# Kernel optimization log

Measured on AMD Instinct MI355X. Metric: run time of the kernel, lower is better.

## Reference

```python
import jax, jax.numpy as jnp
import numpy as np

B, N, T, D = 8, 16, 64, 4
H = 256
N_EDGE_TYPES = 2
BN_EPS = 1e-5


def _rel_matrices(n):
    idx = np.arange(n)
    send, recv = np.meshgrid(idx, idx, indexing='ij')
    mask = send != recv
    eye = np.eye(n, dtype=np.float32)
    return jnp.asarray(eye[recv[mask]]), jnp.asarray(eye[send[mask]])


def _mlp_params(key, n_in, n_hid, n_out):
    k1, k2 = jax.random.split(key)
    s1 = (2.0 / (n_in + n_hid)) ** 0.5
    s2 = (2.0 / (n_hid + n_out)) ** 0.5
    return (jax.random.normal(k1, (n_hid, n_in)) * s1,
            jnp.full((n_hid,), 0.1),
            jax.random.normal(k2, (n_out, n_hid)) * s2,
            jnp.full((n_out,), 0.1),
            jnp.ones((n_out,)),
            jnp.zeros((n_out,)))


def setup_inputs() -> dict:
    key = jax.random.key(0)
    ks = jax.random.split(key, 12)
    rel_rec, rel_send = _rel_matrices(N)
    inp = {
        'inputs': jax.random.normal(ks[0], (B, N, T, D), dtype=jnp.float32),
        'rel_rec': rel_rec,
        'rel_send': rel_send,
    }
    for name, (ni, no), k in [('m1', (D, H), ks[1]), ('m2', (2 * H, H), ks[2]),
                              ('m3', (H, H), ks[3]), ('m4', (3 * H, H), ks[4])]:
        w1, b1, w2, b2, g, be = _mlp_params(k, ni, H, no)
        inp.update({f'{name}_w1': w1, f'{name}_b1': b1, f'{name}_w2': w2,
                    f'{name}_b2': b2, f'{name}_g': g, f'{name}_be': be})
    scale = (1.0 / H) ** 0.5
    inp['lstm_wih'] = jax.random.uniform(ks[5], (3, 4 * H, H), minval=-scale, maxval=scale)
    inp['lstm_whh'] = jax.random.uniform(ks[6], (3, 4 * H, H), minval=-scale, maxval=scale)
    inp['lstm_bih'] = jax.random.uniform(ks[7], (3, 4 * H), minval=-scale, maxval=scale)
    inp['lstm_bhh'] = jax.random.uniform(ks[8], (3, 4 * H), minval=-scale, maxval=scale)
    inp['fco_w'] = jax.random.normal(ks[9], (N_EDGE_TYPES, H)) * (2.0 / (H + N_EDGE_TYPES)) ** 0.5
    inp['fco_b'] = jnp.full((N_EDGE_TYPES,), 0.1)
    return inp


def _mlp(x, w1, b1, w2, b2, g, be):
    h = jax.nn.elu(x @ w1.T + b1)
    h = jax.nn.elu(h @ w2.T + b2)
    # BatchNorm1d (training mode, biased var) over flattened (batch, nodes/edges)
    m = h.mean(axis=(0, 1), keepdims=True)
    v = jnp.mean((h - m) ** 2, axis=(0, 1), keepdims=True)
    return (h - m) * jax.lax.rsqrt(v + BN_EPS) * g + be


def _lstm_layer(x, wih, whh, bih, bhh):
    # x: [BR, T, H]; PyTorch gate order i, f, g, o
    BR = x.shape[0]
    h0 = jnp.zeros((BR, whh.shape[1]), x.dtype)

    def step(carry, xt):
        h, c = carry
        gates = xt @ wih.T + bih + h @ whh.T + bhh
        i, f, g, o = jnp.split(gates, 4, axis=-1)
        c = jax.nn.sigmoid(f) * c + jax.nn.sigmoid(i) * jnp.tanh(g)
        h = jax.nn.sigmoid(o) * jnp.tanh(c)
        return (h, c), h

    (_, _), ys = jax.lax.scan(step, (h0, h0), jnp.swapaxes(x, 0, 1))
    return jnp.swapaxes(ys, 0, 1)


def _node2edge(x, rel_rec, rel_send):
    # rel_*: [E, N], x: [BT, N, H] -> [BT, E, 2H] with (senders, receivers)
    return jnp.concatenate([rel_send @ x, rel_rec @ x], axis=2)


def reference(inputs, rel_rec, rel_send,
              m1_w1, m1_b1, m1_w2, m1_b2, m1_g, m1_be,
              m2_w1, m2_b1, m2_w2, m2_b2, m2_g, m2_be,
              m3_w1, m3_b1, m3_w2, m3_b2, m3_g, m3_be,
              m4_w1, m4_b1, m4_w2, m4_b2, m4_g, m4_be,
              lstm_wih, lstm_whh, lstm_bih, lstm_bhh,
              fco_w, fco_b):
    b, n, t, d = inputs.shape
    x = jnp.transpose(inputs, (0, 2, 1, 3)).reshape(b * t, n, d)
    x = _mlp(x, m1_w1, m1_b1, m1_w2, m1_b2, m1_g, m1_be)          # [BT, N, H]
    x = _node2edge(x, rel_rec, rel_send)                            # [BT, E, 2H]
    x = _mlp(x, m2_w1, m2_b1, m2_w2, m2_b2, m2_g, m2_be)           # [BT, E, H]
    x_skip = x
    # edge2node: rel_rec^T x / N (intended NRI math; source has an arity bug)
    x = jnp.einsum('en,beh->bnh', rel_rec, x) / n                   # [BT, N, H]
    x = _mlp(x, m3_w1, m3_b1, m3_w2, m3_b2, m3_g, m3_be)
    x = _node2edge(x, rel_rec, rel_send)                            # [BT, E, 2H]
    x = jnp.concatenate([x, x_skip], axis=2)                        # [BT, E, 3H]
    x = _mlp(x, m4_w1, m4_b1, m4_w2, m4_b2, m4_g, m4_be)           # [BT, E, H]
    r = x.shape[1]
    x = x.reshape(b, t, r, -1).transpose(0, 2, 1, 3).reshape(b * r, t, -1)
    for layer in range(3):
        x = _lstm_layer(x, lstm_wih[layer], lstm_whh[layer],
                        lstm_bih[layer], lstm_bhh[layer])
    x = x[:, -1, :].reshape(b, r, -1)
    return (x @ fco_w.T + fco_b).reshape(b, r, fco_w.shape[0])
```

## Files before the change

### kernel.cpp

```cpp
#include <hip/hip_runtime.h>


typedef __attribute__((ext_vector_type(4))) float f32x4;
typedef __attribute__((ext_vector_type(8))) _Float16 f16x8;
typedef unsigned long long u64;

#define DEVFN static __device__ __forceinline__

DEVFN float elu_f(float x)  { return x > 0.f ? x : __expf(x) - 1.f; }
DEVFN float sig_f(float x)  { return 1.f / (1.f + __expf(-x)); }
DEVFN float tanh_f(float x) { return 1.f - 2.f / (1.f + __expf(2.f * x)); }

#define M_ID  0
#define M_N2E 1
#define M_M4  2
#define M_L0C 3
#define M_IDC 4

template<int MODE, bool DOELU>
__global__ __launch_bounds__(256) void gemmg(
    const _Float16* __restrict__ A0, const _Float16* __restrict__ A1,
    const float* __restrict__ st0, const float* __restrict__ st1,
    const int* __restrict__ sidx, const int* __restrict__ ridx,
    const _Float16* __restrict__ W, const float* __restrict__ bias,
    _Float16* __restrict__ out, int M, int O, int tc)
{
    constexpr int NSEG = (MODE == M_M4) ? 3 : ((MODE == M_N2E) ? 2 : 1);
    constexpr bool HAS_ST = (MODE == M_N2E) || (MODE == M_M4) || (MODE == M_L0C);
    const int K = NSEG * 256;

    __shared__ _Float16 As[128][40];
    __shared__ _Float16 Ws[128][40];

    const int tid  = threadIdx.x;
    const int lane = tid & 63;
    const int wv   = tid >> 6;
    const int wr   = wv >> 1, wc = wv & 1;
    const int lr   = lane & 15, kg = lane >> 4;
    const int m0   = blockIdx.x * 128;
    const int o0   = blockIdx.y * 128;
    const int srow = tid >> 1;
    const int scol = (tid & 1) * 16;

    const _Float16* ab[3] = {nullptr, nullptr, nullptr};
    const float*   stp[3] = {nullptr, nullptr, nullptr};
    {
        int r = m0 + srow;
        if constexpr (MODE == M_ID) {
            ab[0] = A0 + (size_t)r * 256;
        } else if constexpr (MODE == M_N2E) {
            int bt = r / 240, e = r - bt * 240;
            ab[0] = A0 + (size_t)(bt * 16 + sidx[e]) * 256;
            ab[1] = A0 + (size_t)(bt * 16 + ridx[e]) * 256;
            stp[0] = st0; stp[1] = st0;
        } else if constexpr (MODE == M_M4) {
            int bt = r / 240, e = r - bt * 240;
            ab[0] = A0 + (size_t)(bt * 16 + sidx[e]) * 256;
            ab[1] = A0 + (size_t)(bt * 16 + ridx[e]) * 256;
            ab[2] = A1 + (size_t)r * 256;
            stp[0] = st0; stp[1] = st0; stp[2] = st1;
        } else if constexpr (MODE == M_L0C) {
            int rr = r >> 4, tt = r & 15;
            int b = rr / 240, e = rr - b * 240;
            ab[0] = A0 + (size_t)((b * 64 + tc + tt) * 240 + e) * 256;
            stp[0] = st0;
        } else {
            ab[0] = A0 + (size_t)((r >> 4) * 64 + tc + (r & 15)) * 256;
        }
    }
    const _Float16* wrow = W + (size_t)(o0 + srow) * K;

    f32x4 acc[4][4];
#pragma unroll
    for (int i = 0; i < 4; ++i)
#pragma unroll
        for (int j = 0; j < 4; ++j) acc[i][j] = (f32x4)0.f;

#pragma unroll
    for (int seg = 0; seg < NSEG; ++seg) {
        const _Float16* asrc = ab[seg];
        const float*    st   = stp[seg];
#pragma unroll 1
        for (int kk = 0; kk < 256; kk += 32) {
            f16x8 v0 = *(const f16x8*)(asrc + kk + scol);
            f16x8 v1 = *(const f16x8*)(asrc + kk + scol + 8);
            if constexpr (HAS_ST) {
#pragma unroll
                for (int j = 0; j < 8; ++j) {
                    int c0 = kk + scol + j, c1 = c0 + 8;
                    v0[j] = (_Float16)((float)v0[j] * st[512 + c0] + st[768 + c0]);
                    v1[j] = (_Float16)((float)v1[j] * st[512 + c1] + st[768 + c1]);
                }
            }
            f16x8 w0 = *(const f16x8*)(wrow + seg * 256 + kk + scol);
            f16x8 w1 = *(const f16x8*)(wrow + seg * 256 + kk + scol + 8);
            *(f16x8*)&As[srow][scol]     = v0;
            *(f16x8*)&As[srow][scol + 8] = v1;
            *(f16x8*)&Ws[srow][scol]     = w0;
            *(f16x8*)&Ws[srow][scol + 8] = w1;
            __syncthreads();

            f16x8 af[4], bf[4];
#pragma unroll
            for (int rf = 0; rf < 4; ++rf)
                af[rf] = *(const f16x8*)&As[wr * 64 + rf * 16 + lr][kg * 8];
#pragma unroll
            for (int cf = 0; cf < 4; ++cf)
                bf[cf] = *(const f16x8*)&Ws[wc * 64 + cf * 16 + lr][kg * 8];
#pragma unroll
            for (int rf = 0; rf < 4; ++rf)
#pragma unroll
                for (int cf = 0; cf < 4; ++cf)
                    acc[rf][cf] = __builtin_amdgcn_mfma_f32_16x16x32_f16(
                        af[rf], bf[cf], acc[rf][cf], 0, 0, 0);
            __syncthreads();
        }
    }

#pragma unroll
    for (int rf = 0; rf < 4; ++rf) {
#pragma unroll
        for (int cf = 0; cf < 4; ++cf) {
            int c = o0 + wc * 64 + cf * 16 + lr;
            float bv = bias ? bias[c] : 0.f;
#pragma unroll
            for (int rg = 0; rg < 4; ++rg) {
                int r = m0 + wr * 64 + rf * 16 + kg * 4 + rg;
                float v = acc[rf][cf][rg] + bv;
                if (DOELU) v = elu_f(v);
                out[(size_t)r * O + c] = (_Float16)v;
            }
        }
    }
}

__global__ void mlp1_g1(const float* __restrict__ inp, const float* __restrict__ w1,
                        const float* __restrict__ b1, _Float16* __restrict__ out)
{
    int idx = blockIdx.x * 256 + threadIdx.x;
    int o = idx & 255, row = idx >> 8;
    int bt = row >> 4, n = row & 15, b = bt >> 6, t = bt & 63;
    const float* xp = inp + (((b * 16 + n) * 64 + t) << 2);
    const float* wp = w1 + (o << 2);
    float v = b1[o] + xp[0] * wp[0] + xp[1] * wp[1] + xp[2] * wp[2] + xp[3] * wp[3];
    out[idx] = (_Float16)elu_f(v);
}

__global__ void decode_k(const float* __restrict__ rel_rec, const float* __restrict__ rel_send,
                         int* __restrict__ sidx, int* __restrict__ ridx,
                         int* __restrict__ nodeEdges)
{
    int tid = threadIdx.x;
    if (tid < 240) {
        float as = 0.f, ar = 0.f;
        for (int n = 0; n < 16; ++n) {
            as += rel_send[tid * 16 + n] * (float)n;
            ar += rel_rec[tid * 16 + n] * (float)n;
        }
        sidx[tid] = (int)(as + 0.5f);
        ridx[tid] = (int)(ar + 0.5f);
    }
    __syncthreads();
    if (tid < 16) {
        int k = 0;
        for (int e = 0; e < 240; ++e)
            if (ridx[e] == tid) nodeEdges[tid * 15 + (k++)] = e;
    }
}

__global__ void cvt16(const float* __restrict__ src, _Float16* __restrict__ dst, int n)
{
    int i = blockIdx.x * 256 + threadIdx.x;
    if (i < n) dst[i] = (_Float16)src[i];
}

__global__ void cvtperm(const float* __restrict__ src, _Float16* __restrict__ dst)
{
    int idx = blockIdx.x * 256 + threadIdx.x;
    int k = idx & 255;
    int cp = (idx >> 8) & 1023;
    int l = idx >> 18;
    dst[idx] = (_Float16)src[((size_t)l * 1024 + (cp & 3) * 256 + (cp >> 2)) * 256 + k];
}

__global__ void wprep2(const float* __restrict__ whh, _Float16* __restrict__ W2)
{
    int idx = blockIdx.x * 256 + threadIdx.x;
    int lane = idx & 63; int u = idx >> 6;
    int kc = u & 7; u >>= 3;
    int g  = u & 3; u >>= 2;
    int w  = u & 3; u >>= 2;
    int cq = u & 3; u >>= 2;
    int l  = u;
    int gatecol = g * 256 + cq * 64 + w * 16 + (lane & 15);
    int k = kc * 32 + (lane >> 4) * 8;
    const float* src = whh + (size_t)l * 262144 + (size_t)gatecol * 256 + k;
    f16x8 v;
#pragma unroll
    for (int j = 0; j < 8; ++j) v[j] = (_Float16)src[j];
    *(f16x8*)&W2[(size_t)idx * 8] = v;
}

__global__ void bn_stats(const _Float16* __restrict__ h, float* __restrict__ stats,
                         int Mrows, int rowsPerBlk)
{
    int col = threadIdx.x;
    int r0 = blockIdx.x * rowsPerBlk;
    int r1 = r0 + rowsPerBlk; if (r1 > Mrows) r1 = Mrows;
    float s = 0.f, q = 0.f;
    for (int r = r0; r < r1; ++r) {
        float v = (float)h[(size_t)r * 256 + col];
        s += v; q += v * v;
    }
    atomicAdd(&stats[col], s);
    atomicAdd(&stats[256 + col], q);
}

__global__ void bn_fin(float* __restrict__ stats, const float* __restrict__ g,
                       const float* __restrict__ be, float invM)
{
    int c = threadIdx.x;
    float m  = stats[c] * invM;
    float vr = stats[256 + c] * invM - m * m;
    float sc = rsqrtf(vr + 1e-5f) * g[c];
    stats[512 + c] = sc;
    stats[768 + c] = be[c] - m * sc;
}

__global__ void e2n_k(const _Float16* __restrict__ x2, const float* __restrict__ st,
                      const int* __restrict__ nodeEdges, _Float16* __restrict__ out)
{
    int idx = blockIdx.x * 256 + threadIdx.x;
    int c = (idx & 31) * 8;
    int n = (idx >> 5) & 15;
    int bt = idx >> 9;
    float s[8] = {0, 0, 0, 0, 0, 0, 0, 0};
    for (int k = 0; k < 15; ++k) {
        int e = nodeEdges[n * 15 + k];
        f16x8 v = *(const f16x8*)&x2[(size_t)(bt * 240 + e) * 256 + c];
#pragma unroll
        for (int j = 0; j < 8; ++j) s[j] += (float)v[j];
    }
    f16x8 r;
#pragma unroll
    for (int j = 0; j < 8; ++j)
        r[j] = (_Float16)((st[512 + c + j] * s[j] + 15.f * st[768 + c + j]) * 0.0625f);
    *(f16x8*)&out[(size_t)(bt * 16 + n) * 256 + c] = r;
}

#define STEP(TT, XPU, XPN) do {                                                \
    const int t_ = tc + (TT);                                                  \
    const int ttn_ = ((TT) < 15) ? (TT) + 1 : 15;                              \
    _Pragma("unroll")                                                          \
    for (int rt = 0; rt < 2; ++rt)                                             \
        _Pragma("unroll")                                                      \
        for (int rg = 0; rg < 4; ++rg) {                                       \
            int row = rt * 16 + kg * 4 + rg;                                   \
            XPN[rt * 4 + rg] = *(const u64*)(xwb                               \
                + ((size_t)(r0 + row) * 16 + ttn_) * 1024);                    \
        }                                                                      \
    f32x4 acc[4][2];                                                           \
    _Pragma("unroll")                                                          \
    for (int g = 0; g < 4; ++g)                                                \
        _Pragma("unroll")                                                      \
        for (int rt = 0; rt < 2; ++rt) acc[g][rt] = (f32x4)0.f;                \
    _Pragma("unroll")                                                          \
    for (int kc = 0; kc < 8; ++kc) {                                           \
        const int kb = kc * 64 + kg * 16;                                      \
        const int o0_ = (lr * 512 + kb) ^ ((lr & 7) << 4);                     \
        const int o1_ = ((16 + lr) * 512 + kb) ^ (((16 + lr) & 7) << 4);       \
        f16x8 a0 = *(const f16x8*)(hfulb + o0_);                               \
        f16x8 a1 = *(const f16x8*)(hfulb + o1_);                               \
        _Pragma("unroll")                                                      \
        for (int g = 0; g < 4; ++g) {                                          \
            f16x8 bf = *(const f16x8*)&Wlds[(((w * 4 + g) * 8 + kc) * 64 + lane) * 8]; \
            acc[g][0] = __builtin_amdgcn_mfma_f32_16x16x32_f16(a0, bf, acc[g][0], 0, 0, 0); \
            acc[g][1] = __builtin_amdgcn_mfma_f32_16x16x32_f16(a1, bf, acc[g][1], 0, 0, 0); \
        }                                                                      \
    }                                                                          \
    __syncthreads();                                                           \
    _Float16 hv0[4], hv1[4];                                                   \
    _Pragma("unroll")                                                          \
    for (int rt = 0; rt < 2; ++rt)                                             \
        _Pragma("unroll")                                                      \
        for (int rg = 0; rg < 4; ++rg) {                                       \
            int row = rt * 16 + kg * 4 + rg;                                   \
            union { u64 u; _Float16 h[4]; } xu; xu.u = XPU[rt * 4 + rg];       \
            float gi = acc[0][rt][rg] + (float)xu.h[0] + bs[0];                \
            float gf = acc[1][rt][rg] + (float)xu.h[1] + bs[1];                \
            float gg = acc[2][rt][rg] + (float)xu.h[2] + bs[2];                \
            float go = acc[3][rt][rg] + (float)xu.h[3] + bs[3];                \
            float c  = sig_f(gf) * cst[rt][rg] + sig_f(gi) * tanh_f(gg);       \
            cst[rt][rg] = c;                                                   \
            float h = sig_f(go) * tanh_f(c);                                   \
            _Float16 h16 = (_Float16)h;                                        \
            if (rt == 0) hv0[rg] = h16; else hv1[rg] = h16;                    \
            int off = (row * 512 + col * 2) ^ ((row & 7) << 4);                \
            *(_Float16*)(hfulb + off) = h16;                                   \
        }                                                                      \
    {                                                                          \
        const int lc = w * 16 + lr;                                            \
        union { _Float16 h[4]; u64 u; } pk;                                    \
        pk.h[0] = hv0[0]; pk.h[1] = hv0[1]; pk.h[2] = hv0[2]; pk.h[3] = hv0[3];\
        u64 p0 = pk.u;                                                         \
        pk.h[0] = hv1[0]; pk.h[1] = hv1[1]; pk.h[2] = hv1[2]; pk.h[3] = hv1[3];\
        u64 p1 = pk.u;                                                         \
        u64* hb = hex + ((size_t)fid * 2 + (t_ & 1)) * 512;                    \
        __hip_atomic_store(&hb[(lc * 2 + 0) * 4 + kg], p0,                     \
                           __ATOMIC_RELAXED, __HIP_MEMORY_SCOPE_AGENT);        \
        __hip_atomic_store(&hb[(lc * 2 + 1) * 4 + kg], p1,                     \
                           __ATOMIC_RELAXED, __HIP_MEMORY_SCOPE_AGENT);        \
    }                                                                          \
    __syncthreads();                                                           \
    if (tid == 0)                                                              \
        __hip_atomic_store(&flags[fid], t_ + 1,                                \
                           __ATOMIC_RELEASE, __HIP_MEMORY_SCOPE_AGENT);        \
    if (tid < 3) {                                                             \
        int s = tid + (tid >= colq ? 1 : 0);                                   \
        while (__hip_atomic_load(&flags[rgrp * 4 + s],                         \
                 __ATOMIC_ACQUIRE, __HIP_MEMORY_SCOPE_AGENT) < t_ + 1) {}      \
    }                                                                          \
    __syncthreads();                                                           \
    _Pragma("unroll 1")                                                        \
    for (int i = tid; i < 1536; i += 256) {                                    \
        int sbi = i >> 9;                                                      \
        int sq  = sbi + (sbi >= colq ? 1 : 0);                                 \
        int idx = i & 511;                                                     \
        u64 v = __hip_atomic_load(                                             \
            &hex[(((size_t)rgrp * 4 + sq) * 2 + (t_ & 1)) * 512 + idx],        \
            __ATOMIC_RELAXED, __HIP_MEMORY_SCOPE_AGENT);                       \
        int lc = idx >> 3, rt = (idx >> 2) & 1, k4 = idx & 3;                  \
        int cg = sq * 64 + lc;                                                 \
        union { u64 u; _Float16 h[4]; } un; un.u = v;                          \
        _Pragma("unroll")                                                      \
        for (int rg = 0; rg < 4; ++rg) {                                       \
            int row = rt * 16 + k4 * 4 + rg;                                   \
            int off = (row * 512 + cg * 2) ^ ((row & 7) << 4);                 \
            *(_Float16*)(hfulb + off) = un.h[rg];                              \
        }                                                                      \
    }                                                                          \
    __syncthreads();                                                           \
    {                                                                          \
        int row = tid >> 3, cg = colq * 64 + (tid & 7) * 8;                    \
        int off = (row * 512 + cg * 2) ^ ((row & 7) << 4);                     \
        if (hout) {                                                            \
            f16x8 v = *(const f16x8*)(hfulb + off);                            \
            *(f16x8*)&hout[((size_t)(r0 + row) * 64 + t_) * 256 + cg] = v;     \
        }                                                                      \
        if (hfinal && t_ == 63) {                                              \
            f16x8 v = *(const f16x8*)(hfulb + off);                            \
            *(f16x8*)&hfinal[(size_t)(r0 + row) * 256 + cg] = v;               \
        }                                                                      \
        if ((TT) == 15) {                                                      \
            f16x8 v = *(const f16x8*)(hfulb + off);                            \
            *(f16x8*)&hstate[(size_t)(r0 + row) * 256 + cg] = v;               \
            _Pragma("unroll")                                                  \
            for (int rt = 0; rt < 2; ++rt)                                     \
                _Pragma("unroll")                                              \
                for (int rg = 0; rg < 4; ++rg)                                 \
                    cstate[(size_t)(r0 + rt * 16 + kg * 4 + rg) * 256 + col] = cst[rt][rg]; \
        }                                                                      \
    }                                                                          \
} while (0)

__global__ __launch_bounds__(256) void rec_k(
    const _Float16* __restrict__ xw,
    const _Float16* __restrict__ W2l,
    const float* __restrict__ bih, const float* __restrict__ bhh,
    _Float16* __restrict__ hout,
    _Float16* __restrict__ hfinal,
    u64* __restrict__ hex,
    int* __restrict__ flags,
    int tc,
    _Float16* __restrict__ hstate,
    float* __restrict__ cstate)
{
    __shared__ _Float16 Wlds[65536];
    __shared__ char hfulb[16384];

    const int colq = blockIdx.x >> 6;
    const int rgrp = blockIdx.x & 63;
    if (rgrp >= 60) return;

    const int tid  = threadIdx.x;
    const int lane = tid & 63;
    const int w    = tid >> 6;
    const int lr   = lane & 15, kg = lane >> 4;
    const int fid  = rgrp * 4 + colq;
    const int r0   = rgrp * 32;
    const int col  = colq * 64 + w * 16 + lr;

    {
        const f16x8* src = (const f16x8*)(W2l + (size_t)colq * 65536);
        f16x8* dst = (f16x8*)Wlds;
        for (int i = tid; i < 8192; i += 256) dst[i] = src[i];
    }

    float cst[2][4];
    if (tc == 0) {
        for (int i = tid; i < 2048; i += 256) ((u64*)hfulb)[i] = 0ULL;
#pragma unroll
        for (int rt = 0; rt < 2; ++rt)
#pragma unroll
            for (int rg = 0; rg < 4; ++rg) cst[rt][rg] = 0.f;
    } else {
        for (int i = tid; i < 1024; i += 256) {
            int row = i >> 5, c8 = (i & 31) * 8;
            f16x8 v = *(const f16x8*)&hstate[(size_t)(r0 + row) * 256 + c8];
            int off = (row * 512 + c8 * 2) ^ ((row & 7) << 4);
            *(f16x8*)(hfulb + off) = v;
        }
#pragma unroll
        for (int rt = 0; rt < 2; ++rt)
#pragma unroll
            for (int rg = 0; rg < 4; ++rg)
                cst[rt][rg] = cstate[(size_t)(r0 + rt * 16 + kg * 4 + rg) * 256 + col];
    }

    float bs[4];
#pragma unroll
    for (int g = 0; g < 4; ++g) bs[g] = bih[g * 256 + col] + bhh[g * 256 + col];

    const _Float16* xwb = xw + (size_t)col * 4;

    u64 xpA[8], xpB[8];
#pragma unroll
    for (int rt = 0; rt < 2; ++rt)
#pragma unroll
        for (int rg = 0; rg < 4; ++rg) {
            int row = rt * 16 + kg * 4 + rg;
            xpA[rt * 4 + rg] = *(const u64*)(xwb + (size_t)(r0 + row) * 16 * 1024);
        }
    __syncthreads();

#pragma unroll 1
    for (int it = 0; it < 8; ++it) {
        STEP(it * 2,     xpA, xpB);
        STEP(it * 2 + 1, xpB, xpA);
    }
}

__global__ void fco_k(const _Float16* __restrict__ hout, const float* __restrict__ w,
                      const float* __restrict__ b, float* __restrict__ out)
{
    int row = blockIdx.x;
    int lane = threadIdx.x;
    const _Float16* hp = hout + (size_t)row * 256;
    float s0 = 0.f, s1 = 0.f;
    for (int k = lane; k < 256; k += 64) {
        float v = (float)hp[k];
        s0 += v * w[k];
        s1 += v * w[256 + k];
    }
#pragma unroll
    for (int off = 32; off; off >>= 1) {
        s0 += __shfl_down(s0, off, 64);
        s1 += __shfl_down(s1, off, 64);
    }
    if (lane == 0) {
        out[row * 2 + 0] = s0 + b[0];
        out[row * 2 + 1] = s1 + b[1];
    }
}

extern "C" void kernel_launch(void* const* d_in, const int* in_sizes, int n_in,
                              void* d_out, int out_size, void* d_ws, size_t ws_size,
                              hipStream_t stream)
{
    const float* inputs   = (const float*)d_in[0];
    const float* rel_rec  = (const float*)d_in[1];
    const float* rel_send = (const float*)d_in[2];
    const float *mw1[4], *mb1[4], *mw2[4], *mb2[4], *mg[4], *mbe[4];
    for (int i = 0; i < 4; ++i) {
        mw1[i] = (const float*)d_in[3 + 6 * i + 0];
        mb1[i] = (const float*)d_in[3 + 6 * i + 1];
        mw2[i] = (const float*)d_in[3 + 6 * i + 2];
        mb2[i] = (const float*)d_in[3 + 6 * i + 3];
        mg [i] = (const float*)d_in[3 + 6 * i + 4];
        mbe[i] = (const float*)d_in[3 + 6 * i + 5];
    }
    const float* lstm_wih = (const float*)d_in[27];
    const float* lstm_whh = (const float*)d_in[28];
    const float* lstm_bih = (const float*)d_in[29];
    const float* lstm_bhh = (const float*)d_in[30];
    const float* fco_w    = (const float*)d_in[31];
    const float* fco_b    = (const float*)d_in[32];
    float* out = (float*)d_out;
    (void)in_sizes; (void)n_in; (void)out_size; (void)ws_size;

    char* ws = (char*)d_ws;
    size_t off = 0;
    auto alloc = [&](size_t bytes) -> void* {
        void* p = ws + off;
        off = (off + bytes + 255) & ~(size_t)255;
        return p;
    };

    float* stats    = (float*)alloc(4 * 1024 * 4);
    int*   sidx     = (int*)alloc(240 * 4);
    int*   ridx     = (int*)alloc(240 * 4);
    int*   nodeEdges= (int*)alloc(240 * 4);
    int*   flags    = (int*)alloc(12 * 240 * 4);
    u64*   hexbuf   = (u64*)alloc((size_t)240 * 2 * 512 * 8);

    const int wsz[7] = {65536, 131072, 65536, 65536, 65536, 196608, 65536};
    const float* wsrc[7] = {mw2[0], mw1[1], mw2[1], mw1[2], mw2[2], mw1[3], mw2[3]};
    _Float16* w16[7];
    for (int i = 0; i < 7; ++i) w16[i] = (_Float16*)alloc((size_t)wsz[i] * 2);
    _Float16* wihp = (_Float16*)alloc((size_t)786432 * 2);
    _Float16* W2   = (_Float16*)alloc((size_t)786432 * 2);

    const size_t SM = (size_t)8192 * 256;
    _Float16* h1    = (_Float16*)alloc(SM * 2);
    _Float16* h1b   = (_Float16*)alloc(SM * 2);
    _Float16* xn    = (_Float16*)alloc(SM * 2);
    _Float16* x3h   = (_Float16*)alloc(SM * 2);
    _Float16* x3raw = (_Float16*)alloc(SM * 2);
    _Float16* hfinal= (_Float16*)alloc((size_t)1920 * 256 * 2);
    _Float16* hstate= (_Float16*)alloc((size_t)1920 * 256 * 2);
    float*    cstate= (float*)alloc((size_t)1920 * 256 * 4);

    const size_t BIG = (size_t)122880 * 256;
    _Float16* P  = (_Float16*)alloc(BIG * 2);
    _Float16* Q  = (_Float16*)alloc(BIG * 2);
    _Float16* XW = (_Float16*)alloc((size_t)30720 * 1024 * 2);

    float* st1 = stats, *st2 = stats + 1024, *st3 = stats + 2048, *st4 = stats + 3072;

    auto bn = [&](const _Float16* h, int Mrows, float* st, const float* g, const float* be) {
        hipMemsetAsync(st, 0, 512 * sizeof(float), stream);
        int nblk = (Mrows > 20000) ? 240 : 32;
        int rpb = (Mrows + nblk - 1) / nblk;
        bn_stats<<<nblk, 256, 0, stream>>>(h, st, Mrows, rpb);
        bn_fin<<<1, 256, 0, stream>>>(st, g, be, 1.f / (float)Mrows);
    };

    hipMemsetAsync(flags, 0, 12 * 240 * 4, stream);
    decode_k<<<1, 256, 0, stream>>>(rel_rec, rel_send, sidx, ridx, nodeEdges);
    for (int i = 0; i < 7; ++i)
        cvt16<<<(wsz[i] + 255) / 256, 256, 0, stream>>>(wsrc[i], w16[i], wsz[i]);
    cvtperm<<<3072, 256, 0, stream>>>(lstm_wih, wihp);
    wprep2<<<384, 256, 0, stream>>>(lstm_whh, W2);

    mlp1_g1<<<8192, 256, 0, stream>>>(inputs, mw1[0], mb1[0], h1);
    gemmg<M_ID, true><<<dim3(64, 2), 256, 0, stream>>>(
        h1, nullptr, nullptr, nullptr, sidx, ridx, w16[0], mb2[0], h1b, 8192, 256, 0);
    bn(h1b, 8192, st1, mg[0], mbe[0]);

    gemmg<M_N2E, true><<<dim3(960, 2), 256, 0, stream>>>(
        h1b, nullptr, st1, nullptr, sidx, ridx, w16[1], mb1[1], P, 122880, 256, 0);
    gemmg<M_ID, true><<<dim3(960, 2), 256, 0, stream>>>(
        P, nullptr, nullptr, nullptr, sidx, ridx, w16[2], mb2[1], Q, 122880, 256, 0);
    bn(Q, 122880, st2, mg[1], mbe[1]);

    e2n_k<<<1024, 256, 0, stream>>>(Q, st2, nodeEdges, xn);
    gemmg<M_ID, true><<<dim3(64, 2), 256, 0, stream>>>(
        xn, nullptr, nullptr, nullptr, sidx, ridx, w16[3], mb1[2], x3h, 8192, 256, 0);
    gemmg<M_ID, true><<<dim3(64, 2), 256, 0, stream>>>(
        x3h, nullptr, nullptr, nullptr, sidx, ridx, w16[4], mb2[2], x3raw, 8192, 256, 0);
    bn(x3raw, 8192, st3, mg[2], mbe[2]);

    gemmg<M_M4, true><<<dim3(960, 2), 256, 0, stream>>>(
        x3raw, Q, st3, st2, sidx, ridx, w16[5], mb1[3], P, 122880, 256, 0);
    gemmg<M_ID, true><<<dim3(960, 2), 256, 0, stream>>>(
        P, nullptr, nullptr, nullptr, sidx, ridx, w16[6], mb2[3], Q, 122880, 256, 0);
    bn(Q, 122880, st4, mg[3], mbe[3]);

    for (int l = 0; l < 3; ++l) {
        const _Float16* wih_l = wihp + (size_t)l * 262144;
        const _Float16* W2l   = W2 + (size_t)l * 262144;
        const float* bih_l = lstm_bih + l * 1024;
        const float* bhh_l = lstm_bhh + l * 1024;
        _Float16* hout_l = (l < 2) ? P : nullptr;
        _Float16* hfin_l = (l == 2) ? hfinal : nullptr;
        for (int c = 0; c < 4; ++c) {
            int tc = c * 16;
            if (l == 0)
                gemmg<M_L0C, false><<<dim3(240, 8), 256, 0, stream>>>(
                    Q, nullptr, st4, nullptr, sidx, ridx, wih_l, nullptr,
                    XW, 30720, 1024, tc);
            else
                gemmg<M_IDC, false><<<dim3(240, 8), 256, 0, stream>>>(
                    P, nullptr, nullptr, nullptr, sidx, ridx, wih_l, nullptr,
                    XW, 30720, 1024, tc);
            rec_k<<<256, 256, 0, stream>>>(
                XW, W2l, bih_l, bhh_l, hout_l, hfin_l,
                hexbuf, flags + (l * 4 + c) * 240, tc, hstate, cstate);
        }
    }

    fco_k<<<1920, 64, 0, stream>>>(hfinal, fco_w, fco_b, out);
}
```

Baseline: 3.131 ms.

## Overlap LSTM recurrent cross-block exchange with local-K MMA and double warps

The recurrent LSTM kernel now uses 512 threads, so each wave handles a single 16-row tile instead of two. Each step starts its MMA on the K-chunks it owns locally, using the hidden state this block just produced, before waiting on peer blocks' flags. The peers' hidden-state slices are pulled into LDS only after that, and the remaining chunks are computed afterwards. The hout store moves to the start of the next step and the hstate/cstate saves move out of the loop, which is meant to shorten the serial sync critical path per timestep at the cost of extra barriers and register pressure.

Result: slower. 3.491 ms (+11.5%).

```diff
diff --git a/kernel.cpp b/kernel.cpp
--- a/kernel.cpp
+++ b/kernel.cpp
@@ -248,122 +248,99 @@
     *(f16x8*)&out[(size_t)(bt * 16 + n) * 256 + c] = r;
 }
 
-#define STEP(TT, XPU, XPN) do {                                                \
-    const int t_ = tc + (TT);                                                  \
-    const int ttn_ = ((TT) < 15) ? (TT) + 1 : 15;                              \
+#define MMA_KC(KC) do {                                                        \
+    const int kb_ = (KC) * 64 + kg * 16;                                       \
+    const int ro_ = rt * 16 + lr;                                              \
+    const int o_  = (ro_ * 512 + kb_) ^ ((ro_ & 7) << 4);                      \
+    f16x8 a_ = *(const f16x8*)(hfulb + o_);                                    \
     _Pragma("unroll")                                                          \
-    for (int rt = 0; rt < 2; ++rt)                                             \
+    for (int g_ = 0; g_ < 4; ++g_) {                                           \
+        f16x8 bf_ = *(const f16x8*)&Wlds[(((ws4 * 4 + g_) * 8 + (KC)) * 64 + lane) * 8]; \
+        acc[g_] = __builtin_amdgcn_mfma_f32_16x16x32_f16(a_, bf_, acc[g_], 0, 0, 0); \
+    }                                                                          \
+} while (0)
+
+#define STEP(S, XPU, XPN, FIRSTSTEP) do {                                      \
+    const int t_ = tc + (S);                                                   \
+    if (hout && (S) > 0 && tid < 256) {                                        \
+        int row_ = tid >> 3, c8_ = (tid & 7) * 8;                              \
+        int cg_ = colq * 64 + c8_;                                             \
+        int off_ = (row_ * 512 + cg_ * 2) ^ ((row_ & 7) << 4);                 \
+        f16x8 v_ = *(const f16x8*)(hfulb + off_);                              \
+        *(f16x8*)&hout[((size_t)(r0 + row_) * 64 + (t_ - 1)) * 256 + cg_] = v_;\
+    }                                                                          \
+    {                                                                          \
+        const int ttn_ = ((S) < 15) ? (S) + 1 : 15;                            \
         _Pragma("unroll")                                                      \
-        for (int rg = 0; rg < 4; ++rg) {                                       \
-            int row = rt * 16 + kg * 4 + rg;                                   \
-            XPN[rt * 4 + rg] = *(const u64*)(xwb                               \
-                + ((size_t)(r0 + row) * 16 + ttn_) * 1024);                    \
-        }                                                                      \
-    f32x4 acc[4][2];                                                           \
-    _Pragma("unroll")                                                          \
-    for (int g = 0; g < 4; ++g)                                                \
-        _Pragma("unroll")                                                      \
-        for (int rt = 0; rt < 2; ++rt) acc[g][rt] = (f32x4)0.f;                \
-    _Pragma("unroll")                                                          \
-    for (int kc = 0; kc < 8; ++kc) {                                           \
-        const int kb = kc * 64 + kg * 16;                                      \
-        const int o0_ = (lr * 512 + kb) ^ ((lr & 7) << 4);                     \
-        const int o1_ = ((16 + lr) * 512 + kb) ^ (((16 + lr) & 7) << 4);       \
-        f16x8 a0 = *(const f16x8*)(hfulb + o0_);                               \
-        f16x8 a1 = *(const f16x8*)(hfulb + o1_);                               \
-        _Pragma("unroll")                                                      \
-        for (int g = 0; g < 4; ++g) {                                          \
-            f16x8 bf = *(const f16x8*)&Wlds[(((w * 4 + g) * 8 + kc) * 64 + lane) * 8]; \
-            acc[g][0] = __builtin_amdgcn_mfma_f32_16x16x32_f16(a0, bf, acc[g][0], 0, 0, 0); \
-            acc[g][1] = __builtin_amdgcn_mfma_f32_16x16x32_f16(a1, bf, acc[g][1], 0, 0, 0); \
+        for (int rg_ = 0; rg_ < 4; ++rg_) {                                    \
+            int row_ = rt * 16 + kg * 4 + rg_;                                 \
+            XPN[rg_] = *(const u64*)(xwb + ((size_t)(r0 + row_) * 16 + ttn_) * 1024); \
         }                                                                      \
     }                                                                          \
+    f32x4 acc[4];                                                              \
+    _Pragma("unroll")                                                          \
+    for (int g_ = 0; g_ < 4; ++g_) acc[g_] = (f32x4)0.f;                       \
+    if (FIRSTSTEP) {                                                           \
+        _Pragma("unroll")                                                      \
+        for (int kc_ = 0; kc_ < 8; ++kc_) MMA_KC(kc_);                         \
+    } else {                                                                   \
+        MMA_KC(kco0); MMA_KC(kco0 + 1);                                        \
+        if (tid < 3) {                                                         \
+            int sq_ = tid + (tid >= colq ? 1 : 0);                             \
+            while (__hip_atomic_load(&flags[rgrp * 4 + sq_],                   \
+                     __ATOMIC_ACQUIRE, __HIP_MEMORY_SCOPE_AGENT) < (S)) {}     \
+        }                                                                      \
+        __syncthreads();                                                       \
+        _Pragma("unroll")                                                      \
+        for (int j_ = 0; j_ < 3; ++j_) {                                       \
+            int sq_ = j_ + (j_ >= colq ? 1 : 0);                               \
+            u64 v_ = __hip_atomic_load(                                        \
+                &hex[(((size_t)rgrp * 4 + sq_) * 2 + (((S) - 1) & 1)) * 512 + tid], \
+                __ATOMIC_RELAXED, __HIP_MEMORY_SCOPE_AGENT);                   \
+            int lc_ = tid >> 3, rt_ = (tid >> 2) & 1, kg_ = tid & 3;           \
+            int cg_ = sq_ * 64 + lc_;                                          \
+            union { u64 u; _Float16 h[4]; } un_; un_.u = v_;                   \
+            _Pragma("unroll")                                                  \
+            for (int rg_ = 0; rg_ < 4; ++rg_) {                                \
+                int row_ = rt_ * 16 + kg_ * 4 + rg_;                           \
+                int off_ = (row_ * 512 + cg_ * 2) ^ ((row_ & 7) << 4);         \
+                *(_Float16*)(hfulb + off_) = un_.h[rg_];                       \
+            }                                                                  \
+        }                                                                      \
+        __syncthreads();                                                       \
+        _Pragma("unroll")                                                      \
+        for (int k2_ = 0; k2_ < 6; ++k2_) MMA_KC((kco0 + 2 + k2_) & 7);        \
+    }                                                                          \
     __syncthreads();                                                           \
-    _Float16 hv0[4], hv1[4];                                                   \
-    _Pragma("unroll")                                                          \
-    for (int rt = 0; rt < 2; ++rt)                                             \
+    {                                                                          \
+        _Float16 hv_[4];                                                       \
         _Pragma("unroll")                                                      \
-        for (int rg = 0; rg < 4; ++rg) {                                       \
-            int row = rt * 16 + kg * 4 + rg;                                   \
-            union { u64 u; _Float16 h[4]; } xu; xu.u = XPU[rt * 4 + rg];       \
-            float gi = acc[0][rt][rg] + (float)xu.h[0] + bs[0];                \
-            float gf = acc[1][rt][rg] + (float)xu.h[1] + bs[1];                \
-            float gg = acc[2][rt][rg] + (float)xu.h[2] + bs[2];                \
-            float go = acc[3][rt][rg] + (float)xu.h[3] + bs[3];                \
-            float c  = sig_f(gf) * cst[rt][rg] + sig_f(gi) * tanh_f(gg);       \
-            cst[rt][rg] = c;                                                   \
-            float h = sig_f(go) * tanh_f(c);                                   \
-            _Float16 h16 = (_Float16)h;                                        \
-            if (rt == 0) hv0[rg] = h16; else hv1[rg] = h16;                    \
-            int off = (row * 512 + col * 2) ^ ((row & 7) << 4);                \
-            *(_Float16*)(hfulb + off) = h16;                                   \
+        for (int rg_ = 0; rg_ < 4; ++rg_) {                                    \
+            union { u64 u; _Float16 h[4]; } xu_; xu_.u = XPU[rg_];             \
+            float gi_ = acc[0][rg_] + (float)xu_.h[0] + bs[0];                 \
+            float gf_ = acc[1][rg_] + (float)xu_.h[1] + bs[1];                 \
+            float gg_ = acc[2][rg_] + (float)xu_.h[2] + bs[2];                 \
+            float go_ = acc[3][rg_] + (float)xu_.h[3] + bs[3];                 \
+            float c_  = sig_f(gf_) * cst[rg_] + sig_f(gi_) * tanh_f(gg_);      \
+            cst[rg_] = c_;                                                     \
+            float h_ = sig_f(go_) * tanh_f(c_);                                \
+            hv_[rg_] = (_Float16)h_;                                           \
+            int row_ = rt * 16 + kg * 4 + rg_;                                 \
+            int off_ = (row_ * 512 + col * 2) ^ ((row_ & 7) << 4);             \
+            *(_Float16*)(hfulb + off_) = hv_[rg_];                             \
         }                                                                      \
-    {                                                                          \
-        const int lc = w * 16 + lr;                                            \
-        union { _Float16 h[4]; u64 u; } pk;                                    \
-        pk.h[0] = hv0[0]; pk.h[1] = hv0[1]; pk.h[2] = hv0[2]; pk.h[3] = hv0[3];\
-        u64 p0 = pk.u;                                                         \
-        pk.h[0] = hv1[0]; pk.h[1] = hv1[1]; pk.h[2] = hv1[2]; pk.h[3] = hv1[3];\
-        u64 p1 = pk.u;                                                         \
-        u64* hb = hex + ((size_t)fid * 2 + (t_ & 1)) * 512;                    \
-        __hip_atomic_store(&hb[(lc * 2 + 0) * 4 + kg], p0,                     \
-                           __ATOMIC_RELAXED, __HIP_MEMORY_SCOPE_AGENT);        \
-        __hip_atomic_store(&hb[(lc * 2 + 1) * 4 + kg], p1,                     \
-                           __ATOMIC_RELAXED, __HIP_MEMORY_SCOPE_AGENT);        \
+        union { _Float16 h[4]; u64 u; } pk_;                                   \
+        pk_.h[0] = hv_[0]; pk_.h[1] = hv_[1]; pk_.h[2] = hv_[2]; pk_.h[3] = hv_[3]; \
+        __hip_atomic_store(&hex[((size_t)fid * 2 + ((S) & 1)) * 512 + lc * 8 + rt * 4 + kg], \
+                           pk_.u, __ATOMIC_RELAXED, __HIP_MEMORY_SCOPE_AGENT); \
     }                                                                          \
     __syncthreads();                                                           \
     if (tid == 0)                                                              \
-        __hip_atomic_store(&flags[fid], t_ + 1,                                \
+        __hip_atomic_store(&flags[fid], (S) + 1,                               \
                            __ATOMIC_RELEASE, __HIP_MEMORY_SCOPE_AGENT);        \
-    if (tid < 3) {                                                             \
-        int s = tid + (tid >= colq ? 1 : 0);                                   \
-        while (__hip_atomic_load(&flags[rgrp * 4 + s],                         \
-                 __ATOMIC_ACQUIRE, __HIP_MEMORY_SCOPE_AGENT) < t_ + 1) {}      \
-    }                                                                          \
-    __syncthreads();                                                           \
-    _Pragma("unroll 1")                                                        \
-    for (int i = tid; i < 1536; i += 256) {                                    \
-        int sbi = i >> 9;                                                      \
-        int sq  = sbi + (sbi >= colq ? 1 : 0);                                 \
-        int idx = i & 511;                                                     \
-        u64 v = __hip_atomic_load(                                             \
-            &hex[(((size_t)rgrp * 4 + sq) * 2 + (t_ & 1)) * 512 + idx],        \
-            __ATOMIC_RELAXED, __HIP_MEMORY_SCOPE_AGENT);                       \
-        int lc = idx >> 3, rt = (idx >> 2) & 1, k4 = idx & 3;                  \
-        int cg = sq * 64 + lc;                                                 \
-        union { u64 u; _Float16 h[4]; } un; un.u = v;                          \
-        _Pragma("unroll")                                                      \
-        for (int rg = 0; rg < 4; ++rg) {                                       \
-            int row = rt * 16 + k4 * 4 + rg;                                   \
-            int off = (row * 512 + cg * 2) ^ ((row & 7) << 4);                 \
-            *(_Float16*)(hfulb + off) = un.h[rg];                              \
-        }                                                                      \
-    }                                                                          \
-    __syncthreads();                                                           \
-    {                                                                          \
-        int row = tid >> 3, cg = colq * 64 + (tid & 7) * 8;                    \
-        int off = (row * 512 + cg * 2) ^ ((row & 7) << 4);                     \
-        if (hout) {                                                            \
-            f16x8 v = *(const f16x8*)(hfulb + off);                            \
-            *(f16x8*)&hout[((size_t)(r0 + row) * 64 + t_) * 256 + cg] = v;     \
-        }                                                                      \
-        if (hfinal && t_ == 63) {                                              \
-            f16x8 v = *(const f16x8*)(hfulb + off);                            \
-            *(f16x8*)&hfinal[(size_t)(r0 + row) * 256 + cg] = v;               \
-        }                                                                      \
-        if ((TT) == 15) {                                                      \
-            f16x8 v = *(const f16x8*)(hfulb + off);                            \
-            *(f16x8*)&hstate[(size_t)(r0 + row) * 256 + cg] = v;               \
-            _Pragma("unroll")                                                  \
-            for (int rt = 0; rt < 2; ++rt)                                     \
-                _Pragma("unroll")                                              \
-                for (int rg = 0; rg < 4; ++rg)                                 \
-                    cstate[(size_t)(r0 + rt * 16 + kg * 4 + rg) * 256 + col] = cst[rt][rg]; \
-        }                                                                      \
-    }                                                                          \
 } while (0)
 
-__global__ __launch_bounds__(256) void rec_k(
+__global__ __launch_bounds__(512) void rec_k(
     const _Float16* __restrict__ xw,
     const _Float16* __restrict__ W2l,
     const float* __restrict__ bih, const float* __restrict__ bhh,
@@ -385,36 +362,36 @@
     const int tid  = threadIdx.x;
     const int lane = tid & 63;
     const int w    = tid >> 6;
+    const int ws4  = w & 3;
+    const int rt   = w >> 2;
     const int lr   = lane & 15, kg = lane >> 4;
     const int fid  = rgrp * 4 + colq;
     const int r0   = rgrp * 32;
-    const int col  = colq * 64 + w * 16 + lr;
+    const int lc   = ws4 * 16 + lr;
+    const int col  = colq * 64 + lc;
+    const int kco0 = colq * 2;
 
     {
         const f16x8* src = (const f16x8*)(W2l + (size_t)colq * 65536);
         f16x8* dst = (f16x8*)Wlds;
-        for (int i = tid; i < 8192; i += 256) dst[i] = src[i];
-    }
-
-    float cst[2][4];
+        for (int i = tid; i < 8192; i += 512) dst[i] = src[i];
+    }
+
+    float cst[4];
     if (tc == 0) {
-        for (int i = tid; i < 2048; i += 256) ((u64*)hfulb)[i] = 0ULL;
-#pragma unroll
-        for (int rt = 0; rt < 2; ++rt)
-#pragma unroll
-            for (int rg = 0; rg < 4; ++rg) cst[rt][rg] = 0.f;
+        for (int i = tid; i < 2048; i += 512) ((u64*)hfulb)[i] = 0ULL;
+#pragma unroll
+        for (int rg = 0; rg < 4; ++rg) cst[rg] = 0.f;
     } else {
-        for (int i = tid; i < 1024; i += 256) {
+        for (int i = tid; i < 1024; i += 512) {
             int row = i >> 5, c8 = (i & 31) * 8;
             f16x8 v = *(const f16x8*)&hstate[(size_t)(r0 + row) * 256 + c8];
             int off = (row * 512 + c8 * 2) ^ ((row & 7) << 4);
             *(f16x8*)(hfulb + off) = v;
         }
 #pragma unroll
-        for (int rt = 0; rt < 2; ++rt)
-#pragma unroll
-            for (int rg = 0; rg < 4; ++rg)
-                cst[rt][rg] = cstate[(size_t)(r0 + rt * 16 + kg * 4 + rg) * 256 + col];
+        for (int rg = 0; rg < 4; ++rg)
+            cst[rg] = cstate[(size_t)(r0 + rt * 16 + kg * 4 + rg) * 256 + col];
     }
 
     float bs[4];
@@ -423,21 +400,35 @@
 
     const _Float16* xwb = xw + (size_t)col * 4;
 
-    u64 xpA[8], xpB[8];
-#pragma unroll
-    for (int rt = 0; rt < 2; ++rt)
-#pragma unroll
-        for (int rg = 0; rg < 4; ++rg) {
-            int row = rt * 16 + kg * 4 + rg;
-            xpA[rt * 4 + rg] = *(const u64*)(xwb + (size_t)(r0 + row) * 16 * 1024);
-        }
+    u64 xpA[4], xpB[4];
+#pragma unroll
+    for (int rg = 0; rg < 4; ++rg) {
+        int row = rt * 16 + kg * 4 + rg;
+        xpA[rg] = *(const u64*)(xwb + (size_t)(r0 + row) * 16 * 1024);
+    }
     __syncthreads();
 
 #pragma unroll 1
     for (int it = 0; it < 8; ++it) {
-        STEP(it * 2,     xpA, xpB);
-        STEP(it * 2 + 1, xpB, xpA);
-    }
+        const int s0 = it * 2, s1 = s0 + 1;
+        STEP(s0, xpA, xpB, (it == 0));
+        STEP(s1, xpB, xpA, false);
+    }
+
+    if (tid < 256) {
+        int row = tid >> 3, c8 = (tid & 7) * 8;
+        int cg = colq * 64 + c8;
+        int off = (row * 512 + cg * 2) ^ ((row & 7) << 4);
+        f16x8 v = *(const f16x8*)(hfulb + off);
+        if (hout)
+            *(f16x8*)&hout[((size_t)(r0 + row) * 64 + tc + 15) * 256 + cg] = v;
+        if (hfinal && tc == 48)
+            *(f16x8*)&hfinal[(size_t)(r0 + row) * 256 + cg] = v;
+        *(f16x8*)&hstate[(size_t)(r0 + row) * 256 + cg] = v;
+    }
+#pragma unroll
+    for (int rg = 0; rg < 4; ++rg)
+        cstate[(size_t)(r0 + rt * 16 + kg * 4 + rg) * 256 + col] = cst[rg];
 }
 
 __global__ void fco_k(const _Float16* __restrict__ hout, const float* __restrict__ w,
@@ -583,7 +574,7 @@
                 gemmg<M_IDC, false><<<dim3(240, 8), 256, 0, stream>>>(
                     P, nullptr, nullptr, nullptr, sidx, ridx, wih_l, nullptr,
                     XW, 30720, 1024, tc);
-            rec_k<<<256, 256, 0, stream>>>(
+            rec_k<<<256, 512, 0, stream>>>(
                 XW, W2l, bih_l, bhh_l, hout_l, hfin_l,
                 hexbuf, flags + (l * 4 + c) * 240, tc, hstate, cstate);
         }
```
